# Optimization experiments

Hardware: AMD Instinct MI355X
Metric: run time of the kernel (lower is better)

Reference implementation:

```python
import jax, jax.numpy as jnp
import numpy as np


def setup_inputs() -> dict:
    key = jax.random.key(0)
    k1, k2 = jax.random.split(key)
    # [B, C=1, D, H, W] single-channel 3D volume
    x = jax.random.normal(k1, (8, 1, 128, 128, 128), dtype=jnp.float32)
    # 3x3x3 finite-difference stencil weights (frozen parameter in the original)
    kernel = jax.random.normal(k2, (3, 3, 3), dtype=jnp.float32)
    return {"x": x, "kernel": kernel}


def reference(x, kernel):
    # F.pad(..., 'circular') with pad=1 on each spatial side -> wrap-around pad
    xp = jnp.pad(x, ((0, 0), (0, 0), (1, 1), (1, 1), (1, 1)), mode='wrap')
    # kernel.reshape(1, 1, 3, 3, 3): out_ch=1, in_ch=1 (OIDHW)
    k = kernel.reshape(1, 1, 3, 3, 3)
    # F.conv3d(padding='valid') == cross-correlation, matches lax conv semantics
    out = jax.lax.conv_general_dilated(
        xp, k,
        window_strides=(1, 1, 1),
        padding='VALID',
        dimension_numbers=('NCDHW', 'OIDHW', 'NCDHW'),
    )
    return out  # [8, 1, 128, 128, 128]
```

## Files before the change

### kernel.cpp

```cpp
#include <hip/hip_runtime.h>

#define DIM   128
#define PLANE (DIM*DIM)
#define TD    16

typedef float vfloat4 __attribute__((ext_vector_type(4)));

__global__ __launch_bounds__(256, 4) void conv3d_circ_td16(
    const float* __restrict__ x, const float* __restrict__ kern,
    float* __restrict__ out)
{
    const int tid = threadIdx.x;
    const int bid = blockIdx.x;
    const int b  = bid >> 6;
    const int ht = (bid >> 3) & 7;
    const int dt = bid & 7;
    const int h0 = ht * 16;
    const int d0 = dt * TD;

    const int wq   = (tid & 31) * 4;
    const int hg   = h0 + (tid >> 5) * 2;
    const int lane = tid & 63;
    const int lleft  = (lane & 32) | ((lane - 1) & 31);
    const int lright = (lane & 32) | ((lane + 1) & 31);

    const int ro[4] = {((hg - 1) & (DIM - 1)) * DIM + wq,
                       hg * DIM + wq,
                       ((hg + 1) & (DIM - 1)) * DIM + wq,
                       ((hg + 2) & (DIM - 1)) * DIM + wq};

    float K0[9], K1[9], K2[9];
#pragma unroll
    for (int i = 0; i < 9; ++i) { K0[i] = kern[i]; K1[i] = kern[9 + i]; K2[i] = kern[18 + i]; }

    const float* xb = x + (size_t)b * (DIM * PLANE);
    float* ob = out + (size_t)b * (DIM * PLANE) + (size_t)hg * DIM + wq;

    float rA[4][4], rB[4][4];
    float accA[2][4], accB[2][4];
#pragma unroll
    for (int r = 0; r < 2; ++r)
#pragma unroll
        for (int j = 0; j < 4; ++j) { accA[r][j] = 0.f; accB[r][j] = 0.f; }

#define LOAD(R, P)                                                            \
    {                                                                         \
        const float* xp = xb + (size_t)(((P) & (DIM - 1)) * PLANE);           \
        _Pragma("unroll") for (int rr = 0; rr < 4; ++rr) {                    \
            const vfloat4 a = *(const vfloat4*)(xp + ro[rr]);                 \
            R[rr][0] = a.x; R[rr][1] = a.y; R[rr][2] = a.z; R[rr][3] = a.w;   \
        }                                                                     \
    }

#define STEP(RC, RN, I, DOLOAD)                                               \
    {                                                                         \
        const int p = d0 - 1 + (I);                                           \
        if (DOLOAD) LOAD(RN, p + 1);                                          \
        float e[4][6];                                                        \
        _Pragma("unroll") for (int rr = 0; rr < 4; ++rr) {                    \
            e[rr][0] = __shfl(RC[rr][3], lleft);                 \
            e[rr][1] = RC[rr][0]; e[rr][2] = RC[rr][1];                       \
            e[rr][3] = RC[rr][2]; e[rr][4] = RC[rr][3];                       \
            e[rr][5] = __shfl(RC[rr][0], lright);                \
        }                                                                     \
        float c0[2][4];                                                       \
        _Pragma("unroll") for (int r = 0; r < 2; ++r)                         \
        _Pragma("unroll") for (int j = 0; j < 4; ++j) c0[r][j] = 0.f;         \
        _Pragma("unroll") for (int ch = 0; ch < 3; ++ch)                      \
        _Pragma("unroll") for (int cw = 0; cw < 3; ++cw) {                    \
            const float k0 = K0[ch * 3 + cw];                                 \
            const float k1 = K1[ch * 3 + cw];                                 \
            const float k2 = K2[ch * 3 + cw];                                 \
            _Pragma("unroll") for (int r = 0; r < 2; ++r)                     \
            _Pragma("unroll") for (int j = 0; j < 4; ++j) {                   \
                const float xv = e[r + ch][j + cw];                           \
                accA[r][j] = fmaf(k2, xv, accA[r][j]);                        \
                accB[r][j] = fmaf(k1, xv, accB[r][j]);                        \
                c0[r][j]   = fmaf(k0, xv, c0[r][j]);                          \
            }                                                                 \
        }                                                                     \
        if ((I) >= 2) {                                                       \
            float* op = ob + (size_t)(p - 1) * PLANE;                         \
            _Pragma("unroll") for (int r = 0; r < 2; ++r) {                   \
                vfloat4 v;                                                    \
                v.x = accA[r][0]; v.y = accA[r][1];                           \
                v.z = accA[r][2]; v.w = accA[r][3];                           \
                __builtin_nontemporal_store(v, (vfloat4*)(op + r * DIM));     \
            }                                                                 \
        }                                                                     \
        _Pragma("unroll") for (int r = 0; r < 2; ++r)                        \
        _Pragma("unroll") for (int j = 0; j < 4; ++j)                         \
            { accA[r][j] = accB[r][j]; accB[r][j] = c0[r][j]; }               \
    }

    LOAD(rA, d0 - 1);

#pragma unroll 1
    for (int i = 0; i < 16; i += 2) {
        STEP(rA, rB, i, true);
        STEP(rB, rA, i + 1, true);
    }
    STEP(rA, rB, 16, true);
    STEP(rB, rA, 17, false);
#undef STEP
#undef LOAD
}

extern "C" void kernel_launch(void* const* d_in, const int* in_sizes, int n_in,
                              void* d_out, int out_size, void* d_ws, size_t ws_size,
                              hipStream_t stream) {
    const float* x    = (const float*)d_in[0];
    const float* kern = (const float*)d_in[1];
    float*       out  = (float*)d_out;
    conv3d_circ_td16<<<dim3(512), dim3(256), 0, stream>>>(x, kern, out);
}
```

Baseline: 27.04 us.

## Stream input planes through LDS with async global_load_lds triple buffering

Input depth-planes are now loaded with global_load_lds straight into a per-wave triple-buffered LDS ring. Each plane is fetched two steps ahead and read back with ds_read_b128 after explicit vmcnt waits. Each wave loads its 6-row slab once instead of every thread fetching 4 overlapping rows, which cuts redundant global loads and hides load latency. The cost is extra LDS traffic, hand-written waitcnt counts that must match the store/load interleave, and launch bounds relaxed from 4 to 2 waves per SIMD.

```diff
diff --git a/kernel.cpp b/kernel.cpp
--- a/kernel.cpp
+++ b/kernel.cpp
@@ -5,11 +5,24 @@
 #define TD    16
 
 typedef float vfloat4 __attribute__((ext_vector_type(4)));
+typedef __attribute__((address_space(3))) char as3_char;
+typedef const __attribute__((address_space(1))) char as1_char;
 
-__global__ __launch_bounds__(256, 4) void conv3d_circ_td16(
+#define DSR(d, SBASE, RB) \
+    asm volatile("ds_read_b128 %0, %1 offset:" #RB : "=v"(d) : "v"(SBASE))
+#define WAITVM(N) \
+    asm volatile("s_waitcnt vmcnt(" #N ")" ::: "memory"); \
+    __builtin_amdgcn_sched_barrier(0)
+#define WAITLG \
+    asm volatile("s_waitcnt lgkmcnt(0)" ::: "memory"); \
+    __builtin_amdgcn_sched_barrier(0)
+
+__global__ __launch_bounds__(256, 2) void conv3d_circ_ldsp(
     const float* __restrict__ x, const float* __restrict__ kern,
     float* __restrict__ out)
 {
+    __shared__ char smem[4 * 3 * 3072];
+
     const int tid = threadIdx.x;
     const int bid = blockIdx.x;
     const int b  = bid >> 6;
@@ -18,50 +31,66 @@
     const int h0 = ht * 16;
     const int d0 = dt * TD;
 
-    const int wq   = (tid & 31) * 4;
+    const int wv   = tid >> 6;
+    const int lane = tid & 63;
+    const int hp   = (tid >> 5) & 1;
+    const int wq   = (lane & 31) * 4;
     const int hg   = h0 + (tid >> 5) * 2;
-    const int lane = tid & 63;
     const int lleft  = (lane & 32) | ((lane - 1) & 31);
     const int lright = (lane & 32) | ((lane + 1) & 31);
+    const int rbase  = h0 + 4 * wv - 1;
 
-    const int ro[4] = {((hg - 1) & (DIM - 1)) * DIM + wq,
-                       hg * DIM + wq,
-                       ((hg + 1) & (DIM - 1)) * DIM + wq,
-                       ((hg + 2) & (DIM - 1)) * DIM + wq};
+    int goff[3];
+#pragma unroll
+    for (int k = 0; k < 3; ++k) {
+        const int u = k * 64 + lane;
+        goff[k] = (((rbase + (u >> 5)) & (DIM - 1)) * DIM) + ((u & 31) * 4);
+    }
+
+    as3_char* lwave = (as3_char*)smem + wv * 9216;
+    const int rd_base = (int)(size_t)((as3_char*)smem)
+                      + wv * 9216 + hp * 1024 + (lane & 31) * 16;
+    const int sb0 = rd_base, sb1 = rd_base + 3072, sb2 = rd_base + 6144;
 
     float K0[9], K1[9], K2[9];
 #pragma unroll
     for (int i = 0; i < 9; ++i) { K0[i] = kern[i]; K1[i] = kern[9 + i]; K2[i] = kern[18 + i]; }
 
     const float* xb = x + (size_t)b * (DIM * PLANE);
-    float* ob = out + (size_t)b * (DIM * PLANE) + (size_t)hg * DIM + wq;
+    float* optr = out + (size_t)b * (DIM * PLANE) + (size_t)d0 * PLANE
+                + (size_t)hg * DIM + wq;
 
-    float rA[4][4], rB[4][4];
+    vfloat4 cur[4];
     float accA[2][4], accB[2][4];
 #pragma unroll
     for (int r = 0; r < 2; ++r)
 #pragma unroll
         for (int j = 0; j < 4; ++j) { accA[r][j] = 0.f; accB[r][j] = 0.f; }
 
-#define LOAD(R, P)                                                            \
+#define GLOAD(SLOT, PP)                                                       \
     {                                                                         \
-        const float* xp = xb + (size_t)(((P) & (DIM - 1)) * PLANE);           \
-        _Pragma("unroll") for (int rr = 0; rr < 4; ++rr) {                    \
-            const vfloat4 a = *(const vfloat4*)(xp + ro[rr]);                 \
-            R[rr][0] = a.x; R[rr][1] = a.y; R[rr][2] = a.z; R[rr][3] = a.w;   \
-        }                                                                     \
+        const float* xp_ = xb + (size_t)(((PP) & (DIM - 1)) * PLANE);         \
+        _Pragma("unroll") for (int k = 0; k < 3; ++k)                         \
+            __builtin_amdgcn_global_load_lds(                                 \
+                (as1_char*)(const char*)(xp_ + goff[k]),                      \
+                (as3_char*)(lwave + (SLOT) * 3072 + k * 1024), 16, 0, 0);     \
     }
 
-#define STEP(RC, RN, I, DOLOAD)                                               \
+#define STEP(RS, WS, VM, DOLOAD, DOSTORE)                                     \
     {                                                                         \
-        const int p = d0 - 1 + (I);                                           \
-        if (DOLOAD) LOAD(RN, p + 1);                                          \
+        if (DOLOAD) GLOAD(WS, p + 2);                                         \
+        WAITVM(VM);                                                           \
+        DSR(cur[0], sb##RS, 0);                                               \
+        DSR(cur[1], sb##RS, 512);                                             \
+        DSR(cur[2], sb##RS, 1024);                                            \
+        DSR(cur[3], sb##RS, 1536);                                            \
+        WAITLG;                                                               \
         float e[4][6];                                                        \
         _Pragma("unroll") for (int rr = 0; rr < 4; ++rr) {                    \
-            e[rr][0] = __shfl(RC[rr][3], lleft);                 \
-            e[rr][1] = RC[rr][0]; e[rr][2] = RC[rr][1];                       \
-            e[rr][3] = RC[rr][2]; e[rr][4] = RC[rr][3];                       \
-            e[rr][5] = __shfl(RC[rr][0], lright);                \
+            e[rr][0] = __shfl(cur[rr][3], lleft);                             \
+            e[rr][1] = cur[rr][0]; e[rr][2] = cur[rr][1];                     \
+            e[rr][3] = cur[rr][2]; e[rr][4] = cur[rr][3];                     \
+            e[rr][5] = __shfl(cur[rr][0], lright);                            \
         }                                                                     \
         float c0[2][4];                                                       \
         _Pragma("unroll") for (int r = 0; r < 2; ++r)                         \
@@ -79,31 +108,38 @@
                 c0[r][j]   = fmaf(k0, xv, c0[r][j]);                          \
             }                                                                 \
         }                                                                     \
-        if ((I) >= 2) {                                                       \
-            float* op = ob + (size_t)(p - 1) * PLANE;                         \
+        if (DOSTORE) {                                                        \
             _Pragma("unroll") for (int r = 0; r < 2; ++r) {                   \
                 vfloat4 v;                                                    \
                 v.x = accA[r][0]; v.y = accA[r][1];                           \
                 v.z = accA[r][2]; v.w = accA[r][3];                           \
-                __builtin_nontemporal_store(v, (vfloat4*)(op + r * DIM));     \
+                __builtin_nontemporal_store(v, (vfloat4*)(optr + r * DIM));   \
             }                                                                 \
+            optr += PLANE;                                                    \
         }                                                                     \
         _Pragma("unroll") for (int r = 0; r < 2; ++r)                        \
         _Pragma("unroll") for (int j = 0; j < 4; ++j)                         \
             { accA[r][j] = accB[r][j]; accB[r][j] = c0[r][j]; }               \
+        ++p;                                                                  \
     }
 
-    LOAD(rA, d0 - 1);
-
+    int p = d0 - 1;
+    GLOAD(0, d0 - 1);
+    GLOAD(1, d0);
+    STEP(0, 2, 6,  true,  false);
+    STEP(1, 0, 6,  true,  false);
+    STEP(2, 1, 6,  true,  true );
+    STEP(0, 2, 8,  true,  true );
 #pragma unroll 1
-    for (int i = 0; i < 16; i += 2) {
-        STEP(rA, rB, i, true);
-        STEP(rB, rA, i + 1, true);
+    for (int j = 0; j < 4; ++j) {
+        STEP(1, 0, 10, true, true);
+        STEP(2, 1, 10, true, true);
+        STEP(0, 2, 10, true, true);
     }
-    STEP(rA, rB, 16, true);
-    STEP(rB, rA, 17, false);
+    STEP(1, 0, 7,  false, true );
+    STEP(2, 0, 4,  false, true );
 #undef STEP
-#undef LOAD
+#undef GLOAD
 }
 
 extern "C" void kernel_launch(void* const* d_in, const int* in_sizes, int n_in,
@@ -112,5 +148,5 @@
     const float* x    = (const float*)d_in[0];
     const float* kern = (const float*)d_in[1];
     float*       out  = (float*)d_out;
-    conv3d_circ_td16<<<dim3(512), dim3(256), 0, stream>>>(x, kern, out);
+    conv3d_circ_ldsp<<<dim3(512), dim3(256), 0, stream>>>(x, kern, out);
 }
```

Result: slower. 28.83 us (+6.6%).
